# Optimization experiments

Measured on AMD Instinct MI355X. Metric: run time of the kernel, lower is better.

Reference implementation:

```python
import jax, jax.numpy as jnp
import numpy as np

KERNEL = 7
STRIDE = 3
C_IN, C_OUT = 3, 4
HIDDEN, OUTPUT = 64, 10
H_OUT = (32 - KERNEL) // STRIDE + 1  # 9
FC1_IN = C_OUT * H_OUT * H_OUT       # 324


def setup_inputs() -> dict:
    key = jax.random.key(0)
    ks = jax.random.split(key, 6)
    B = 16384
    x = jax.random.normal(ks[0], (B, C_IN, 32, 32), dtype=jnp.float32)
    conv_w = jax.random.normal(ks[1], (C_OUT, C_IN, KERNEL, KERNEL), dtype=jnp.float32) * 0.05
    fc1_w = jax.random.normal(ks[2], (HIDDEN, FC1_IN), dtype=jnp.float32) * (1.0 / np.sqrt(FC1_IN))
    fc1_b = jax.random.normal(ks[3], (HIDDEN,), dtype=jnp.float32) * 0.01
    fc2_w = jax.random.normal(ks[4], (OUTPUT, HIDDEN), dtype=jnp.float32) * (1.0 / np.sqrt(HIDDEN))
    fc2_b = jax.random.normal(ks[5], (OUTPUT,), dtype=jnp.float32) * 0.01
    return {"x": x, "conv_w": conv_w, "fc1_w": fc1_w, "fc1_b": fc1_b, "fc2_w": fc2_w, "fc2_b": fc2_b}


def reference(x, conv_w, fc1_w, fc1_b, fc2_w, fc2_b):
    # conv (NO bias, matching original forward which only uses conv1.weight)
    y = jax.lax.conv_general_dilated(
        x, conv_w, window_strides=(STRIDE, STRIDE), padding='VALID',
        dimension_numbers=('NCHW', 'OIHW', 'NCHW'))  # [B, 4, 9, 9]
    y = y * y
    y = y.reshape(y.shape[0], -1)                    # [B, 324]
    h = y @ fc1_w.T + fc1_b                          # [B, 64]
    h = h * h
    out = h @ fc2_w.T + fc2_b                        # [B, 10]
    return out
```

## Files before the change

### kernel.cpp

```cpp
#include <hip/hip_runtime.h>
#include <string.h>


typedef _Float16 f16;
typedef f16 f16x8 __attribute__((ext_vector_type(8)));
typedef __fp16 fp16x2 __attribute__((ext_vector_type(2)));
typedef float f32x4 __attribute__((ext_vector_type(4)));

#define NS     32
#define YS_B   13824
#define LDS_B  (13824 + NS * 720)

__device__ __forceinline__ unsigned pack_rtz(float a, float b) {
    fp16x2 h = __builtin_amdgcn_cvt_pkrtz(a, b);
    unsigned u; memcpy(&u, &h, 4); return u;
}

__device__ __forceinline__ void write_half(f16* wptr, const float4 ldv[5], int half) {
    unsigned h[10];
#pragma unroll
    for (int i = 0; i < 5; ++i) {
        h[2*i]   = pack_rtz(ldv[i].x, ldv[i].y);
        h[2*i+1] = pack_rtz(ldv[i].z, ldv[i].w);
    }
    const int owb = half * 4;
    if (!half) {
        uint4 v; v.x = h[0]; v.y = h[1]; v.z = h[2]; v.w = h[3];
        *reinterpret_cast<uint4*>(wptr) = v;
    }
    {
        uint4 v;
        v.x = __builtin_amdgcn_alignbit(h[2], h[1], 16);
        v.y = __builtin_amdgcn_alignbit(h[3], h[2], 16);
        v.z = __builtin_amdgcn_alignbit(h[4], h[3], 16);
        v.w = __builtin_amdgcn_alignbit(h[5], h[4], 16);
        *reinterpret_cast<uint4*>(wptr + (owb + 1) * 8) = v;
    }
    {
        uint4 v; v.x = h[3]; v.y = h[4]; v.z = h[5]; v.w = h[6];
        *reinterpret_cast<uint4*>(wptr + (owb + 2) * 8) = v;
    }
    {
        uint4 v;
        v.x = __builtin_amdgcn_alignbit(h[5], h[4], 16);
        v.y = __builtin_amdgcn_alignbit(h[6], h[5], 16);
        v.z = __builtin_amdgcn_alignbit(h[7], h[6], 16);
        v.w = __builtin_amdgcn_alignbit(h[8], h[7], 16);
        *reinterpret_cast<uint4*>(wptr + (owb + 3) * 8) = v;
    }
    {
        uint4 v; v.x = h[6]; v.y = h[7]; v.z = h[8]; v.w = h[9];
        *reinterpret_cast<uint4*>(wptr + (owb + 4) * 8) = v;
    }
}

__global__ __launch_bounds__(256, 2) void convnet_mfma(
    const float* __restrict__ x,
    const float* __restrict__ cw,
    const float* __restrict__ fc1w,
    const float* __restrict__ fc1b,
    const float* __restrict__ fc2w,
    const float* __restrict__ fc2b,
    float* __restrict__ out)
{
    __shared__ unsigned char lds[LDS_B];
    f16* WINH = (f16*)lds;
    f16* YS   = (f16*)(lds + YS_B);
    float* HSQ = (float*)lds;

    const int t    = threadIdx.x;
    const int lane = t & 63;
    const int w    = t >> 6;
    const int g    = lane >> 4;
    const int lr   = lane & 15;
    const size_t base_s = (size_t)blockIdx.x * NS;

    f16x8 wcf[6];
#pragma unroll
    for (int st = 0; st < 6; ++st) {
        f16x8 v = {0, 0, 0, 0, 0, 0, 0, 0};
        int seg = st * 4 + g;
        if (lr < 4 && seg <= 20) {
            int ci = seg >= 14 ? 2 : (seg >= 7 ? 1 : 0);
            int kh = seg - ci * 7;
            const float* wr = cw + ((lr * 3 + ci) * 7 + kh) * 7;
#pragma unroll
            for (int j = 0; j < 7; ++j) v[j] = (f16)wr[j];
        }
        wcf[st] = v;
    }

    int seg2off[6];
#pragma unroll
    for (int st = 0; st < 6; ++st) {
        int seg  = st * 4 + g;
        int segc = seg > 20 ? 20 : seg;
        int ci   = segc >= 14 ? 2 : (segc >= 7 ? 1 : 0);
        int kh   = segc - ci * 7;
        seg2off[st] = ci * 4608 + kh * 144;
    }

    const int u = 3 - w;
    const int ntiles = (u < 2) ? 2 : 1;
    int rowbase[2], pbase[2];
#pragma unroll
    for (int ti = 0; ti < 2; ++ti) {
        int tile = u + ti * 4;
        int tc   = tile > 5 ? 5 : tile;
        int grow = tc * 16 + lr;
        int p    = grow > 80 ? 80 : grow;
        int oh   = (p * 57) >> 9;
        int ow   = p - oh * 9;
        rowbase[ti] = oh * 432 + ow * 16;
        pbase[ti]   = tc * 16 + g * 4;
    }

    const bool stg  = t < 192;
    const int  r_   = t >> 1;
    const int  half = t & 1;
    const int  sci  = r_ >> 5;
    const int  srow = r_ & 31;
    const int  goff = sci * 1024 + srow * 32 + (half ? 12 : 0);
    f16* wptr = WINH + sci * 2304 + srow * 72;

    float4 ldv[5];
    if (stg) {
        const float* gp = x + base_s * 3072 + goff;
#pragma unroll
        for (int i = 0; i < 5; ++i) ldv[i] = *(const float4*)(gp + 4 * i);
    }
#pragma unroll
    for (int i = 0; i < 3; ++i) {
        int idx = i * 256 + t;
        if (idx < NS * 18) {
            int si = idx / 18, d = idx - si * 18;
            *(unsigned*)(YS + si * 360 + 324 + d * 2) = 0u;
        }
    }
    if (stg) write_half(wptr, ldv, half);
    __syncthreads();

    for (int s = 0; s < NS; ++s) {
        if (s < NS - 1 && stg) {
            const float* gp = x + (base_s + s + 1) * 3072 + goff;
#pragma unroll
            for (int i = 0; i < 5; ++i) ldv[i] = *(const float4*)(gp + 4 * i);
        }
        f16* ysp = YS + s * 360;
        __builtin_amdgcn_s_setprio(1);
#pragma unroll
        for (int ti = 0; ti < 2; ++ti) {
            if (ti < ntiles) {
                const unsigned char* pA = lds + rowbase[ti];
                f32x4 acc = {0.f, 0.f, 0.f, 0.f};
#pragma unroll
                for (int st = 0; st < 6; ++st) {
                    f16x8 af = *(const f16x8*)(pA + seg2off[st]);
                    acc = __builtin_amdgcn_mfma_f32_16x16x32_f16(af, wcf[st], acc, 0, 0, 0);
                }
                if (lr < 4) {
#pragma unroll
                    for (int r = 0; r < 4; ++r) {
                        int p = pbase[ti] + r;
                        if (p < 81) {
                            float y = acc[r];
                            ysp[lr * 81 + p] = (f16)(y * y);
                        }
                    }
                }
            }
        }
        __builtin_amdgcn_s_setprio(0);
        __syncthreads();
        if (s < NS - 1) {
            if (stg) write_half(wptr, ldv, half);
            __syncthreads();
        }
    }

    {
        f32x4 a0 = {0.f, 0.f, 0.f, 0.f};
        f32x4 a1 = {0.f, 0.f, 0.f, 0.f};
        const int n = w * 16 + lr;
        const float* w1r = fc1w + n * 324;
        __builtin_amdgcn_s_setprio(1);
#pragma unroll
        for (int st = 0; st < 10; ++st) {
            f16x8 av0 = *(const f16x8*)(YS +        lr  * 360 + st * 32 + g * 8);
            f16x8 av1 = *(const f16x8*)(YS + (16 + lr) * 360 + st * 32 + g * 8);
            float4 v0 = *(const float4*)(w1r + st * 32 + g * 8);
            float4 v1 = *(const float4*)(w1r + st * 32 + g * 8 + 4);
            float vv[8] = {v0.x, v0.y, v0.z, v0.w, v1.x, v1.y, v1.z, v1.w};
            f16x8 bh, bl;
#pragma unroll
            for (int j = 0; j < 8; ++j) {
                f16 hi = (f16)vv[j];
                bh[j] = hi;
                bl[j] = (f16)(vv[j] - (float)hi);
            }
            a0 = __builtin_amdgcn_mfma_f32_16x16x32_f16(av0, bh, a0, 0, 0, 0);
            a0 = __builtin_amdgcn_mfma_f32_16x16x32_f16(av0, bl, a0, 0, 0, 0);
            a1 = __builtin_amdgcn_mfma_f32_16x16x32_f16(av1, bh, a1, 0, 0, 0);
            a1 = __builtin_amdgcn_mfma_f32_16x16x32_f16(av1, bl, a1, 0, 0, 0);
        }
        {
            f16x8 av0 = *(const f16x8*)(YS +        lr  * 360 + 320 + g * 8);
            f16x8 av1 = *(const f16x8*)(YS + (16 + lr) * 360 + 320 + g * 8);
            f16x8 bh = {0,0,0,0,0,0,0,0}, bl = {0,0,0,0,0,0,0,0};
            if (g == 0) {
                float4 v0 = *(const float4*)(w1r + 320);
                float vv[4] = {v0.x, v0.y, v0.z, v0.w};
#pragma unroll
                for (int j = 0; j < 4; ++j) {
                    f16 hi = (f16)vv[j];
                    bh[j] = hi;
                    bl[j] = (f16)(vv[j] - (float)hi);
                }
            }
            a0 = __builtin_amdgcn_mfma_f32_16x16x32_f16(av0, bh, a0, 0, 0, 0);
            a0 = __builtin_amdgcn_mfma_f32_16x16x32_f16(av0, bl, a0, 0, 0, 0);
            a1 = __builtin_amdgcn_mfma_f32_16x16x32_f16(av1, bh, a1, 0, 0, 0);
            a1 = __builtin_amdgcn_mfma_f32_16x16x32_f16(av1, bl, a1, 0, 0, 0);
        }
        __builtin_amdgcn_s_setprio(0);
        float bias = fc1b[n];
#pragma unroll
        for (int r = 0; r < 4; ++r) {
            int s0 = g * 4 + r;
            float h0 = a0[r] + bias;
            HSQ[s0 * 65 + n] = h0 * h0;
            float h1 = a1[r] + bias;
            HSQ[(s0 + 16) * 65 + n] = h1 * h1;
        }
    }
    __syncthreads();

#pragma unroll
    for (int b = 0; b < 2; ++b) {
        int idx = b * 256 + t;
        if (idx < NS * 10) {
            int sj = idx / 10, j = idx - sj * 10;
            float a = fc2b[j];
            const float* wr = fc2w + j * 64;
            const float* hv = &HSQ[sj * 65];
#pragma unroll
            for (int i = 0; i < 64; ++i) a += wr[i] * hv[i];
            out[(base_s + sj) * 10 + j] = a;
        }
    }
}

extern "C" void kernel_launch(void* const* d_in, const int* in_sizes, int n_in,
                              void* d_out, int out_size, void* d_ws, size_t ws_size,
                              hipStream_t stream) {
    const float* x    = (const float*)d_in[0];
    const float* cw   = (const float*)d_in[1];
    const float* fc1w = (const float*)d_in[2];
    const float* fc1b = (const float*)d_in[3];
    const float* fc2w = (const float*)d_in[4];
    const float* fc2b = (const float*)d_in[5];
    float* out = (float*)d_out;

    const int B = in_sizes[0] / 3072;
    hipLaunchKernelGGL(convnet_mfma, dim3(B / NS), dim3(256), 0, stream,
                       x, cw, fc1w, fc1b, fc2w, fc2b, out);
}
```

Before: 41.55 us.

## Overlap first-half FC1 MFMA with conv loop iterations

Computes the FC1 product for the first 16 samples inside the conv sample loop (iterations 17-27), once their conv outputs are in LDS, so only the second 16 samples remain for the tail. HSQ moves to its own LDS region so it no longer aliases the input window buffer that is still in use. This is meant to shorten the serial FC1 epilogue by interleaving its MFMA and global weight loads with conv work. In exchange it uses more LDS, which may reduce occupancy, and keeps the a0 accumulator live through the loop, which adds register pressure.

```diff
diff --git a/kernel.cpp b/kernel.cpp
--- a/kernel.cpp
+++ b/kernel.cpp
@@ -9,7 +9,8 @@
 
 #define NS     32
 #define YS_B   13824
-#define LDS_B  (13824 + NS * 720)
+#define HSQ_B  (13824 + NS * 720)
+#define LDS_B  (HSQ_B + NS * 65 * 4)
 
 __device__ __forceinline__ unsigned pack_rtz(float a, float b) {
     fp16x2 h = __builtin_amdgcn_cvt_pkrtz(a, b);
@@ -51,6 +52,16 @@
     {
         uint4 v; v.x = h[6]; v.y = h[7]; v.z = h[8]; v.w = h[9];
         *reinterpret_cast<uint4*>(wptr + (owb + 4) * 8) = v;
+    }
+}
+
+__device__ __forceinline__ void split8(float4 v0, float4 v1, f16x8& bh, f16x8& bl) {
+    float vv[8] = {v0.x, v0.y, v0.z, v0.w, v1.x, v1.y, v1.z, v1.w};
+#pragma unroll
+    for (int j = 0; j < 8; ++j) {
+        f16 hi = (f16)vv[j];
+        bh[j] = hi;
+        bl[j] = (f16)(vv[j] - (float)hi);
     }
 }
 
@@ -64,9 +75,9 @@
     float* __restrict__ out)
 {
     __shared__ unsigned char lds[LDS_B];
-    f16* WINH = (f16*)lds;
-    f16* YS   = (f16*)(lds + YS_B);
-    float* HSQ = (float*)lds;
+    f16* WINH  = (f16*)lds;
+    f16* YS    = (f16*)(lds + YS_B);
+    float* HSQ = (float*)(lds + HSQ_B);
 
     const int t    = threadIdx.x;
     const int lane = t & 63;
@@ -123,6 +134,10 @@
     const int  goff = sci * 1024 + srow * 32 + (half ? 12 : 0);
     f16* wptr = WINH + sci * 2304 + srow * 72;
 
+    const int n = w * 16 + lr;
+    const float* w1r = fc1w + n * 324;
+    f32x4 a0 = {0.f, 0.f, 0.f, 0.f};
+
     float4 ldv[5];
     if (stg) {
         const float* gp = x + base_s * 3072 + goff;
@@ -171,6 +186,36 @@
             }
         }
         __builtin_amdgcn_s_setprio(0);
+
+        {
+            int ks = s - 17;
+            if (ks >= 0 && ks < 11) {
+                if (ks < 10) {
+                    f16x8 av = *(const f16x8*)(YS + lr * 360 + ks * 32 + g * 8);
+                    float4 v0 = *(const float4*)(w1r + ks * 32 + g * 8);
+                    float4 v1 = *(const float4*)(w1r + ks * 32 + g * 8 + 4);
+                    f16x8 bh, bl;
+                    split8(v0, v1, bh, bl);
+                    a0 = __builtin_amdgcn_mfma_f32_16x16x32_f16(av, bh, a0, 0, 0, 0);
+                    a0 = __builtin_amdgcn_mfma_f32_16x16x32_f16(av, bl, a0, 0, 0, 0);
+                } else {
+                    f16x8 av = *(const f16x8*)(YS + lr * 360 + 320 + g * 8);
+                    f16x8 bh = {0,0,0,0,0,0,0,0}, bl = {0,0,0,0,0,0,0,0};
+                    if (g == 0) {
+                        float4 v0 = *(const float4*)(w1r + 320);
+                        float vv[4] = {v0.x, v0.y, v0.z, v0.w};
+#pragma unroll
+                        for (int j = 0; j < 4; ++j) {
+                            f16 hi = (f16)vv[j];
+                            bh[j] = hi;
+                            bl[j] = (f16)(vv[j] - (float)hi);
+                        }
+                    }
+                    a0 = __builtin_amdgcn_mfma_f32_16x16x32_f16(av, bh, a0, 0, 0, 0);
+                    a0 = __builtin_amdgcn_mfma_f32_16x16x32_f16(av, bl, a0, 0, 0, 0);
+                }
+            }
+        }
         __syncthreads();
         if (s < NS - 1) {
             if (stg) write_half(wptr, ldv, half);
@@ -179,33 +224,20 @@
     }
 
     {
-        f32x4 a0 = {0.f, 0.f, 0.f, 0.f};
         f32x4 a1 = {0.f, 0.f, 0.f, 0.f};
-        const int n = w * 16 + lr;
-        const float* w1r = fc1w + n * 324;
         __builtin_amdgcn_s_setprio(1);
 #pragma unroll
         for (int st = 0; st < 10; ++st) {
-            f16x8 av0 = *(const f16x8*)(YS +        lr  * 360 + st * 32 + g * 8);
-            f16x8 av1 = *(const f16x8*)(YS + (16 + lr) * 360 + st * 32 + g * 8);
+            f16x8 av = *(const f16x8*)(YS + (16 + lr) * 360 + st * 32 + g * 8);
             float4 v0 = *(const float4*)(w1r + st * 32 + g * 8);
             float4 v1 = *(const float4*)(w1r + st * 32 + g * 8 + 4);
-            float vv[8] = {v0.x, v0.y, v0.z, v0.w, v1.x, v1.y, v1.z, v1.w};
             f16x8 bh, bl;
-#pragma unroll
-            for (int j = 0; j < 8; ++j) {
-                f16 hi = (f16)vv[j];
-                bh[j] = hi;
-                bl[j] = (f16)(vv[j] - (float)hi);
-            }
-            a0 = __builtin_amdgcn_mfma_f32_16x16x32_f16(av0, bh, a0, 0, 0, 0);
-            a0 = __builtin_amdgcn_mfma_f32_16x16x32_f16(av0, bl, a0, 0, 0, 0);
-            a1 = __builtin_amdgcn_mfma_f32_16x16x32_f16(av1, bh, a1, 0, 0, 0);
-            a1 = __builtin_amdgcn_mfma_f32_16x16x32_f16(av1, bl, a1, 0, 0, 0);
+            split8(v0, v1, bh, bl);
+            a1 = __builtin_amdgcn_mfma_f32_16x16x32_f16(av, bh, a1, 0, 0, 0);
+            a1 = __builtin_amdgcn_mfma_f32_16x16x32_f16(av, bl, a1, 0, 0, 0);
         }
         {
-            f16x8 av0 = *(const f16x8*)(YS +        lr  * 360 + 320 + g * 8);
-            f16x8 av1 = *(const f16x8*)(YS + (16 + lr) * 360 + 320 + g * 8);
+            f16x8 av = *(const f16x8*)(YS + (16 + lr) * 360 + 320 + g * 8);
             f16x8 bh = {0,0,0,0,0,0,0,0}, bl = {0,0,0,0,0,0,0,0};
             if (g == 0) {
                 float4 v0 = *(const float4*)(w1r + 320);
@@ -217,20 +249,16 @@
                     bl[j] = (f16)(vv[j] - (float)hi);
                 }
             }
-            a0 = __builtin_amdgcn_mfma_f32_16x16x32_f16(av0, bh, a0, 0, 0, 0);
-            a0 = __builtin_amdgcn_mfma_f32_16x16x32_f16(av0, bl, a0, 0, 0, 0);
-            a1 = __builtin_amdgcn_mfma_f32_16x16x32_f16(av1, bh, a1, 0, 0, 0);
-            a1 = __builtin_amdgcn_mfma_f32_16x16x32_f16(av1, bl, a1, 0, 0, 0);
+            a1 = __builtin_amdgcn_mfma_f32_16x16x32_f16(av, bh, a1, 0, 0, 0);
+            a1 = __builtin_amdgcn_mfma_f32_16x16x32_f16(av, bl, a1, 0, 0, 0);
         }
         __builtin_amdgcn_s_setprio(0);
         float bias = fc1b[n];
 #pragma unroll
         for (int r = 0; r < 4; ++r) {
             int s0 = g * 4 + r;
-            float h0 = a0[r] + bias;
-            HSQ[s0 * 65 + n] = h0 * h0;
-            float h1 = a1[r] + bias;
-            HSQ[(s0 + 16) * 65 + n] = h1 * h1;
+            float h0 = a0[r] + bias; HSQ[ s0       * 65 + n] = h0 * h0;
+            float h1 = a1[r] + bias; HSQ[(s0 + 16) * 65 + n] = h1 * h1;
         }
     }
     __syncthreads();
```

New measurement: 46.97 us. +13.0%, slower.
